# Kernel tuning notes

Measured on AMD Instinct MI355X. Metric: run time of the kernel, lower is better.

Reference implementation:

```python
import jax, jax.numpy as jnp
import numpy as np

B, S, D, H = 8, 1025, 768, 12
HD = D // H  # 64

def setup_inputs() -> dict:
    key = jax.random.key(0)
    ks = jax.random.split(key, 5)
    scale = 0.02
    return {
        "hidden_states": jax.random.normal(ks[0], (B, S, D), jnp.float32),
        "rel_bias": jax.random.normal(ks[1], (1, H, S, S), jnp.float32),
        "Wq": jax.random.normal(ks[2], (D, D), jnp.float32) * scale,
        "bq": jnp.zeros((D,), jnp.float32),
        "Wk": jax.random.normal(ks[3], (D, D), jnp.float32) * scale,
        "bk": jnp.zeros((D,), jnp.float32),
        "Wv": jax.random.normal(ks[4], (D, D), jnp.float32) * scale,
        "bv": jnp.zeros((D,), jnp.float32),
    }

def reference(hidden_states, rel_bias, Wq, bq, Wk, bk, Wv, bv):
    b, s, d = hidden_states.shape
    def split_heads(t):  # [B,S,D] -> [B,H,S,hd]
        return t.reshape(b, s, H, HD).transpose(0, 2, 1, 3)
    q = split_heads(hidden_states @ Wq + bq)
    k = split_heads(hidden_states @ Wk + bk)
    v = split_heads(hidden_states @ Wv + bv)
    inv_sqrt_hd = 1.0 / jnp.sqrt(jnp.asarray(HD, q.dtype))
    scores = jnp.einsum("bhqd,bhkd->bhqk", q, k) * inv_sqrt_hd
    scores = scores + rel_bias  # broadcast [1,H,S,S]
    probs = jax.nn.softmax(scores, axis=-1)
    ctx = jnp.einsum("bhqk,bhkd->bhqd", probs, v)
    out = ctx.transpose(0, 2, 1, 3).reshape(b, s, d)
    return out
```

## Files before the change

kernel.cpp:

```cpp
#include <hip/hip_runtime.h>

using f32x4  = __attribute__((ext_vector_type(4))) float;
using bf16x8 = __attribute__((ext_vector_type(8))) short;

#define SEQ 1025
#define NH  12

__device__ __forceinline__ unsigned short f2bf(float f) {
  unsigned u = __float_as_uint(f);
  u += 0x7FFFu + ((u >> 16) & 1u);
  return (unsigned short)(u >> 16);
}

__device__ __forceinline__ unsigned short f2bf_p(float f) {
  return (unsigned short)((__float_as_uint(f) + 0x8000u) >> 16);
}

__device__ __forceinline__ void async16(const void* g, void* s) {
  __builtin_amdgcn_global_load_lds(
      (const __attribute__((address_space(1))) void*)g,
      (__attribute__((address_space(3))) void*)s, 16, 0, 0);
}


__device__ __forceinline__ void conv_x_body(int bx, const float* __restrict__ X,
                                            ushort* __restrict__ Xb) {
  int t = bx * 256 + threadIdx.x;
  if (t >= 8320 * 96) return;
  int row = t / 96;
  size_t e = (size_t)t * 8;
  union { uint4 q; ushort us[8]; } o;
  if (row < 8200) {
    float4 f0 = *(const float4*)(X + e);
    float4 f1 = *(const float4*)(X + e + 4);
    o.us[0] = f2bf(f0.x); o.us[1] = f2bf(f0.y); o.us[2] = f2bf(f0.z); o.us[3] = f2bf(f0.w);
    o.us[4] = f2bf(f1.x); o.us[5] = f2bf(f1.y); o.us[6] = f2bf(f1.z); o.us[7] = f2bf(f1.w);
  } else {
    o.q = make_uint4(0, 0, 0, 0);
  }
  *(uint4*)(Xb + e) = o.q;
}

__device__ __forceinline__ void pack_w_body(int j, const float* __restrict__ Wq,
                                            const float* __restrict__ Wk,
                                            const float* __restrict__ Wv,
                                            ushort* __restrict__ Wt,
                                            const float* __restrict__ bq,
                                            const float* __restrict__ bk,
                                            const float* __restrict__ bv,
                                            float* __restrict__ bc,
                                            float (*tile)[33]) {
  const int nt = j % 72;
  const int kt = j / 72;
  if (kt == 0 && nt < 9) {
    int t2 = nt * 256 + threadIdx.x;
    if (t2 < 768) bc[t2] = bq[t2];
    else if (t2 < 1536) bc[t2] = bk[t2 - 768];
    else if (t2 < 2304) bc[t2] = bv[t2 - 1536];
  }
  const int sel = nt / 24;
  const int o0 = (nt - sel * 24) * 32;
  const int k0 = kt * 32;
  const float* W = sel == 0 ? Wq : sel == 1 ? Wk : Wv;
  const int t = threadIdx.x;
  const int x = t & 31, y = t >> 5;
  for (int p = 0; p < 4; ++p)
    tile[y + p * 8][x] = W[(size_t)(k0 + y + p * 8) * 768 + o0 + x];
  __syncthreads();
  for (int p = 0; p < 4; ++p) {
    const int nl = y + p * 8;
    Wt[(size_t)(nt * 32 + nl) * 768 + k0 + x] = f2bf(tile[x][nl]);
  }
}

__device__ __forceinline__ void repack_body(int id, const float* __restrict__ rel,
                                            float* __restrict__ bf,
                                            float (*lds)[580]) {
  const int half = id & 1;
  const int hw = id >> 1;
  const int h = hw / 72, w = hw - h * 72;
  const int t = threadIdx.x;
  const int W = half ? 512 : 576;
  const int cbase = half * 576;
  const float* src = rel + (size_t)h * SEQ * SEQ;
  for (int r = 0; r < 16; ++r) {
    int q = w * 16 + r; if (q > 1024) q = 1024;
    const float* row = src + (size_t)q * SEQ;
    for (int c = t; c < W; c += 256) {
      int col = cbase + c;
      lds[r][c] = (col <= 1024) ? row[col] * 1.44269504f : -3.0e30f;
    }
  }
  __syncthreads();
  const int lane = t >> 2, ct = t & 3;
  const int l16 = lane & 15, quad = lane >> 4;
  const int nkt = half ? 8 : 9;
  for (int ktl = 0; ktl < nkt; ++ktl) {
    const int kt = half * 9 + ktl;
    const int col = ktl * 64 + ct * 16 + l16;
    f32x4 v;
    v[0] = lds[quad * 4 + 0][col];
    v[1] = lds[quad * 4 + 1][col];
    v[2] = lds[quad * 4 + 2][col];
    v[3] = lds[quad * 4 + 3][col];
    *(f32x4*)(bf + (((size_t)h * 17 + kt) * 72 + w) * 1024 + lane * 16 + ct * 4) = v;
  }
}

__device__ __forceinline__ void gemm_body(int mb, int nb,
                                          const ushort* __restrict__ A,
                                          const ushort* __restrict__ Bt,
                                          const float* __restrict__ bias,
                                          ushort* __restrict__ Qo,
                                          ushort* __restrict__ Ko,
                                          ushort* __restrict__ Vo,
                                          char* smem) {
  ushort* a_sm = (ushort*)smem;
  ushort* b_sm = (ushort*)(smem + 8192);
  ushort* c_sm = (ushort*)(smem + 16384);
  const int t = threadIdx.x;
  const int lane = t & 63, wave = t >> 6;
  const int quad = lane >> 4, l16 = lane & 15;
  const int wrow = wave >> 1, wcol = wave & 1;
  const int m0 = mb * 128, n0 = nb * 128;

  f32x4 acc[4][4] = {};

  const ushort* a_g = A + (size_t)m0 * 768;
  const ushort* b_g = Bt + (size_t)n0 * 768;

  for (int k0 = 0; k0 < 768; k0 += 32) {
    __syncthreads();
    for (int r = 0; r < 2; ++r) {
      int c = r * 256 + t;
      int row = c >> 2;
      int colb = (c & 3) * 16;
      async16((const char*)(a_g + (size_t)row * 768 + k0) + colb, (char*)a_sm + c * 16);
      async16((const char*)(b_g + (size_t)row * 768 + k0) + colb, (char*)b_sm + c * 16);
    }
    __syncthreads();
    bf16x8 af[4], bfr[4];
    for (int i = 0; i < 4; ++i) {
      af[i]  = *(const bf16x8*)(a_sm + (wrow * 64 + i * 16 + l16) * 32 + quad * 8);
      bfr[i] = *(const bf16x8*)(b_sm + (wcol * 64 + i * 16 + l16) * 32 + quad * 8);
    }
    for (int i = 0; i < 4; ++i)
      for (int j = 0; j < 4; ++j)
        acc[i][j] = __builtin_amdgcn_mfma_f32_16x16x32_bf16(af[i], bfr[j], acc[i][j], 0, 0, 0);
  }

  const int sel = n0 / 768;
  const int o0 = n0 - sel * 768;
  const int hh0 = o0 >> 6;
  ushort* dst = sel == 0 ? Qo : sel == 1 ? Ko : Vo;
  float bvj[4];
  for (int j = 0; j < 4; ++j) bvj[j] = bias[n0 + wcol * 64 + j * 16 + l16];

  for (int p = 0; p < 2; ++p) {
    __syncthreads();
    if (wrow == p) {
      for (int i = 0; i < 4; ++i)
        for (int j = 0; j < 4; ++j)
          for (int r = 0; r < 4; ++r)
            c_sm[(i * 16 + quad * 4 + r) * 136 + wcol * 64 + j * 16 + l16] =
                f2bf(acc[i][j][r] + bvj[j]);
    }
    __syncthreads();
    const int head = t >> 7;
    const int ci = t & 127;
    for (int k = 0; k < 4; ++k) {
      int ch = ci + 128 * k;
      int row = ch >> 3, off = (ch & 7) * 8;
      int gm = m0 + p * 64 + row;
      if (gm < 8200) {
        int bb = gm / 1025, ss = gm - bb * 1025;
        uint4 v = *(const uint4*)(c_sm + row * 136 + head * 64 + off);
        *(uint4*)(dst + (((size_t)(bb * NH + hh0 + head) * SEQ + ss) << 6) + off) = v;
      }
    }
  }
}


__global__ __launch_bounds__(256) void prep(const float* __restrict__ X,
                                            ushort* __restrict__ Xb,
                                            const float* __restrict__ Wq,
                                            const float* __restrict__ Wk,
                                            const float* __restrict__ Wv,
                                            ushort* __restrict__ Wt,
                                            const float* __restrict__ bq,
                                            const float* __restrict__ bk,
                                            const float* __restrict__ bv,
                                            float* __restrict__ bc) {
  __shared__ __align__(16) float tile[32][33];
  const int bx = blockIdx.x;
  if (bx < 3120) conv_x_body(bx, X, Xb);
  else pack_w_body(bx - 3120, Wq, Wk, Wv, Wt, bq, bk, bv, bc, tile);
}

__global__ __launch_bounds__(256, 3) void gemm_repack(
    const ushort* __restrict__ A, const ushort* __restrict__ Bt,
    const float* __restrict__ biasc, ushort* __restrict__ Qo,
    ushort* __restrict__ Ko, ushort* __restrict__ Vo,
    const float* __restrict__ rel, float* __restrict__ bf) {
  __shared__ __align__(16) char smem[37120];
  const int bx = blockIdx.x;
  const int g = bx / 56, r = bx - g * 56;
  if (r < 24) {
    const int s = g * 24 + r;
    const int x = s & 7, k = s >> 3;
    const int ml = k / 18, n = k - ml * 18;
    int m;
    if (x == 0) m = ml;
    else { if (ml >= 8) return; m = 9 + (x - 1) * 8 + ml; }
    gemm_body(m, n, A, Bt, biasc, Qo, Ko, Vo, smem);
  } else {
    repack_body(g * 32 + (r - 24), rel, bf, (float(*)[580])smem);
  }
}

__global__ __launch_bounds__(256) void gemm_qkv_k(const ushort* __restrict__ A,
                                                  const ushort* __restrict__ Bt,
                                                  const float* __restrict__ biasc,
                                                  ushort* __restrict__ Qo,
                                                  ushort* __restrict__ Ko,
                                                  ushort* __restrict__ Vo) {
  __shared__ __align__(16) char smem[33792];
  gemm_body(blockIdx.x, blockIdx.y, A, Bt, biasc, Qo, Ko, Vo, smem);
}

__global__ __launch_bounds__(256, 4) void repack_k(const float* __restrict__ rel,
                                                   float* __restrict__ bf) {
  __shared__ __align__(16) float lds[16][580];
  repack_body(blockIdx.x, rel, bf, lds);
}

__global__ __launch_bounds__(256, 4) void attn(const ushort* __restrict__ Qb,
                                               const ushort* __restrict__ Kb,
                                               const ushort* __restrict__ Vb,
                                               const float* __restrict__ biasF,
                                               float* __restrict__ out) {
  __shared__ __align__(16) char smem[36864];
  ushort* p_sm = (ushort*)smem;
  ushort* k_sm = (ushort*)(smem + 18432);
  ushort* v_sm = (ushort*)(smem + 27648);

  const int t = threadIdx.x;
  const int lane = t & 63, wave = t >> 6;
  const int quad = lane >> 4, l16 = lane & 15;

  const int id = blockIdx.x;
  const int x = id & 7, s = id >> 3;
  const int Gg = s / 9, qt = s - Gg * 9;
  const int G = Gg * 8 + x;
  const int b = G / 12, h = G - b * 12;
  const int q0 = qt * 128;

  const size_t bh = (size_t)(b * NH + h) * SEQ * 64;
  const ushort* Qp = Qb + bh;
  const ushort* Kp = Kb + bh;
  const ushort* Vp = Vb + bh;

  uint4 kpre0, kpre1, vpre0, vpre1;
  const int vkp2 = t & 31, vhb = (t >> 5) * 8;

  auto issue_kv = [&](int kb) {
    {
      int c = t, row = c >> 3, cb = (c & 7) * 8;
      int rk = kb + row; if (rk > 1024) rk = 1024;
      kpre0 = *(const uint4*)(Kp + (size_t)rk * 64 + cb);
    }
    {
      int c = t + 256, row = c >> 3, cb = (c & 7) * 8;
      int rk = kb + row; if (rk > 1024) rk = 1024;
      kpre1 = *(const uint4*)(Kp + (size_t)rk * 64 + cb);
    }
    {
      int r0 = kb + vkp2 * 2;
      int r0c = r0 > 1024 ? 1024 : r0;
      int r1c = r0 + 1 > 1024 ? 1024 : r0 + 1;
      vpre0 = *(const uint4*)(Vp + (size_t)r0c * 64 + vhb);
      vpre1 = *(const uint4*)(Vp + (size_t)r1c * 64 + vhb);
    }
  };

  issue_kv(0);

  ushort* pw = p_sm + wave * (32 * 72);
  const int qbase = q0 + wave * 32;
  for (int i = 0; i < 4; ++i) {
    int c = lane + 64 * i;
    int row = c >> 3, cb = (c & 7) * 8;
    int rq = qbase + row; if (rq > 1024) rq = 1024;
    *(uint4*)(pw + row * 72 + cb) = *(const uint4*)(Qp + (size_t)rq * 64 + cb);
  }
  bf16x8 qf[2][2];
  for (int rt = 0; rt < 2; ++rt)
    for (int ks = 0; ks < 2; ++ks)
      qf[rt][ks] = *(const bf16x8*)(pw + (rt * 16 + l16) * 72 + ks * 32 + quad * 8);

  float lst[8] = {0, 0, 0, 0, 0, 0, 0, 0};
  f32x4 oacc[2][4] = {};
  const float c_scale = 0.18033688f;
  const float* bf_base = biasF +
      ((size_t)h * 17 * 72 + (qt * 8 + wave * 2)) * 1024 + (lane << 4);

  for (int kt = 0; kt < 17; ++kt) {
    __syncthreads();
    {
      int c = t;
      *(uint4*)(k_sm + (c >> 3) * 72 + (c & 7) * 8) = kpre0;
      c = t + 256;
      *(uint4*)(k_sm + (c >> 3) * 72 + (c & 7) * 8) = kpre1;
    }
    {
      union { uint4 q; ushort us[8]; } e0, e1;
      e0.q = vpre0; e1.q = vpre1;
      for (int e = 0; e < 8; ++e)
        *(unsigned*)(v_sm + (vhb + e) * 72 + vkp2 * 2) =
            (unsigned)e0.us[e] | ((unsigned)e1.us[e] << 16);
    }
    __syncthreads();

    const float* bfp = bf_base + (size_t)kt * (72 * 1024);
    f32x4 br[2][4];
    for (int rt = 0; rt < 2; ++rt)
      for (int ct = 0; ct < 4; ++ct)
        br[rt][ct] = *(const f32x4*)(bfp + rt * 1024 + ct * 4);

    if (kt < 16) issue_kv(kt * 64 + 64);

    f32x4 sc[2][4] = {};
    for (int ct = 0; ct < 4; ++ct)
      for (int ks = 0; ks < 2; ++ks) {
        bf16x8 kf = *(const bf16x8*)(k_sm + (ct * 16 + l16) * 72 + ks * 32 + quad * 8);
        sc[0][ct] = __builtin_amdgcn_mfma_f32_16x16x32_bf16(qf[0][ks], kf, sc[0][ct], 0, 0, 0);
        sc[1][ct] = __builtin_amdgcn_mfma_f32_16x16x32_bf16(qf[1][ks], kf, sc[1][ct], 0, 0, 0);
      }

    for (int rt = 0; rt < 2; ++rt)
      for (int ct = 0; ct < 4; ++ct)
        for (int r2 = 0; r2 < 4; ++r2) {
          float p = __builtin_amdgcn_exp2f(
              fmaf(sc[rt][ct][r2], c_scale, br[rt][ct][r2]));
          lst[rt * 4 + r2] += p;
          pw[(rt * 16 + quad * 4 + r2) * 72 + ct * 16 + l16] = f2bf_p(p);
        }

    for (int ks = 0; ks < 2; ++ks) {
      bf16x8 pf0 = *(const bf16x8*)(pw + l16 * 72 + ks * 32 + quad * 8);
      bf16x8 pf1 = *(const bf16x8*)(pw + (16 + l16) * 72 + ks * 32 + quad * 8);
      for (int c4 = 0; c4 < 4; ++c4) {
        bf16x8 vf = *(const bf16x8*)(v_sm + (c4 * 16 + l16) * 72 + ks * 32 + quad * 8);
        oacc[0][c4] = __builtin_amdgcn_mfma_f32_16x16x32_bf16(pf0, vf, oacc[0][c4], 0, 0, 0);
        oacc[1][c4] = __builtin_amdgcn_mfma_f32_16x16x32_bf16(pf1, vf, oacc[1][c4], 0, 0, 0);
      }
    }
  }

  for (int si = 0; si < 8; ++si) {
    float s2 = lst[si];
    s2 += __shfl_xor(s2, 1);
    s2 += __shfl_xor(s2, 2);
    s2 += __shfl_xor(s2, 4);
    s2 += __shfl_xor(s2, 8);
    lst[si] = s2;
  }
  for (int rt = 0; rt < 2; ++rt)
    for (int r2 = 0; r2 < 4; ++r2) {
      int sr = qbase + rt * 16 + quad * 4 + r2;
      if (sr < SEQ) {
        float inv = 1.0f / lst[rt * 4 + r2];
        float* op = out + ((size_t)b * SEQ + sr) * 768 + h * 64;
        for (int c4 = 0; c4 < 4; ++c4)
          op[c4 * 16 + l16] = oacc[rt][c4][r2] * inv;
      }
    }
}

extern "C" void kernel_launch(void* const* d_in, const int* in_sizes, int n_in,
                              void* d_out, int out_size, void* d_ws, size_t ws_size,
                              hipStream_t stream) {
  const float* X  = (const float*)d_in[0];
  const float* rb = (const float*)d_in[1];
  const float* Wq = (const float*)d_in[2];
  const float* bq = (const float*)d_in[3];
  const float* Wk = (const float*)d_in[4];
  const float* bk = (const float*)d_in[5];
  const float* Wv = (const float*)d_in[6];
  const float* bv = (const float*)d_in[7];
  float* out = (float*)d_out;
  char* ws = (char*)d_ws;

  ushort* Qb    = (ushort*)ws;
  ushort* Kb    = (ushort*)(ws + 12595200);
  ushort* Vb    = (ushort*)(ws + 25190400);
  ushort* Xb    = (ushort*)(ws + 37785600);
  ushort* Wt    = (ushort*)(ws + 50565120);
  float*  biasc = (float*)(ws + 54104064);

  const bool bigws = ws_size >= 114275328ULL;
  float* biasF = bigws ? (float*)(ws + 54113280) : (float*)(ws + 37785600);

  prep<<<3120 + 1728, 256, 0, stream>>>(X, Xb, Wq, Wk, Wv, Wt, bq, bk, bv, biasc);
  if (bigws) {
    gemm_repack<<<3024, 256, 0, stream>>>(Xb, Wt, biasc, Qb, Kb, Vb, rb, biasF);
  } else {
    gemm_qkv_k<<<dim3(65, 18), 256, 0, stream>>>(Xb, Wt, biasc, Qb, Kb, Vb);
    repack_k<<<NH * 72 * 2, 256, 0, stream>>>(rb, biasF);
  }
  attn<<<864, 256, 0, stream>>>(Qb, Kb, Vb, biasF, out);
}
```

Measured before the change: 308.9 us.

## Split fused prep/gemm-repack kernels and remap attention blocks for L2 locality

Undoes the fused prep and gemm+repack kernels and launches conv_x, pack_w, repack_k and a swizzled gemm_x as separate kernels. The attention block-to-(batch, head, q-tile) mapping is reordered so that consecutive blocks share a head's bias slice across batches, with a tail remap for the remaining tiles. The aim is better L2 reuse of the bias tensor in attention and simpler kernels, at the cost of extra launches and the lost overlap between the GEMM and the bias repack.

```diff
diff --git a/kernel.cpp b/kernel.cpp
--- a/kernel.cpp
+++ b/kernel.cpp
@@ -23,9 +23,9 @@
 }
 
 
-__device__ __forceinline__ void conv_x_body(int bx, const float* __restrict__ X,
-                                            ushort* __restrict__ Xb) {
-  int t = bx * 256 + threadIdx.x;
+__global__ __launch_bounds__(256) void conv_x(const float* __restrict__ X,
+                                              ushort* __restrict__ Xb) {
+  int t = blockIdx.x * 256 + threadIdx.x;
   if (t >= 8320 * 96) return;
   int row = t / 96;
   size_t e = (size_t)t * 8;
@@ -41,15 +41,16 @@
   *(uint4*)(Xb + e) = o.q;
 }
 
-__device__ __forceinline__ void pack_w_body(int j, const float* __restrict__ Wq,
-                                            const float* __restrict__ Wk,
-                                            const float* __restrict__ Wv,
-                                            ushort* __restrict__ Wt,
-                                            const float* __restrict__ bq,
-                                            const float* __restrict__ bk,
-                                            const float* __restrict__ bv,
-                                            float* __restrict__ bc,
-                                            float (*tile)[33]) {
+__global__ __launch_bounds__(256) void pack_w(const float* __restrict__ Wq,
+                                              const float* __restrict__ Wk,
+                                              const float* __restrict__ Wv,
+                                              ushort* __restrict__ Wt,
+                                              const float* __restrict__ bq,
+                                              const float* __restrict__ bk,
+                                              const float* __restrict__ bv,
+                                              float* __restrict__ bc) {
+  __shared__ __align__(16) float tile[32][33];
+  const int j = blockIdx.x;
   const int nt = j % 72;
   const int kt = j / 72;
   if (kt == 0 && nt < 9) {
@@ -73,9 +74,10 @@
   }
 }
 
-__device__ __forceinline__ void repack_body(int id, const float* __restrict__ rel,
-                                            float* __restrict__ bf,
-                                            float (*lds)[580]) {
+__global__ __launch_bounds__(256, 4) void repack_k(const float* __restrict__ rel,
+                                                   float* __restrict__ bf) {
+  __shared__ __align__(16) float lds[16][580];
+  const int id = blockIdx.x;
   const int half = id & 1;
   const int hw = id >> 1;
   const int h = hw / 72, w = hw - h * 72;
@@ -181,58 +183,20 @@
   }
 }
 
-
-__global__ __launch_bounds__(256) void prep(const float* __restrict__ X,
-                                            ushort* __restrict__ Xb,
-                                            const float* __restrict__ Wq,
-                                            const float* __restrict__ Wk,
-                                            const float* __restrict__ Wv,
-                                            ushort* __restrict__ Wt,
-                                            const float* __restrict__ bq,
-                                            const float* __restrict__ bk,
-                                            const float* __restrict__ bv,
-                                            float* __restrict__ bc) {
-  __shared__ __align__(16) float tile[32][33];
-  const int bx = blockIdx.x;
-  if (bx < 3120) conv_x_body(bx, X, Xb);
-  else pack_w_body(bx - 3120, Wq, Wk, Wv, Wt, bq, bk, bv, bc, tile);
-}
-
-__global__ __launch_bounds__(256, 3) void gemm_repack(
-    const ushort* __restrict__ A, const ushort* __restrict__ Bt,
-    const float* __restrict__ biasc, ushort* __restrict__ Qo,
-    ushort* __restrict__ Ko, ushort* __restrict__ Vo,
-    const float* __restrict__ rel, float* __restrict__ bf) {
-  __shared__ __align__(16) char smem[37120];
-  const int bx = blockIdx.x;
-  const int g = bx / 56, r = bx - g * 56;
-  if (r < 24) {
-    const int s = g * 24 + r;
-    const int x = s & 7, k = s >> 3;
-    const int ml = k / 18, n = k - ml * 18;
-    int m;
-    if (x == 0) m = ml;
-    else { if (ml >= 8) return; m = 9 + (x - 1) * 8 + ml; }
-    gemm_body(m, n, A, Bt, biasc, Qo, Ko, Vo, smem);
-  } else {
-    repack_body(g * 32 + (r - 24), rel, bf, (float(*)[580])smem);
-  }
-}
-
-__global__ __launch_bounds__(256) void gemm_qkv_k(const ushort* __restrict__ A,
-                                                  const ushort* __restrict__ Bt,
-                                                  const float* __restrict__ biasc,
-                                                  ushort* __restrict__ Qo,
-                                                  ushort* __restrict__ Ko,
-                                                  ushort* __restrict__ Vo) {
+__global__ __launch_bounds__(256) void gemm_x(const ushort* __restrict__ A,
+                                              const ushort* __restrict__ Bt,
+                                              const float* __restrict__ biasc,
+                                              ushort* __restrict__ Qo,
+                                              ushort* __restrict__ Ko,
+                                              ushort* __restrict__ Vo) {
   __shared__ __align__(16) char smem[33792];
-  gemm_body(blockIdx.x, blockIdx.y, A, Bt, biasc, Qo, Ko, Vo, smem);
-}
-
-__global__ __launch_bounds__(256, 4) void repack_k(const float* __restrict__ rel,
-                                                   float* __restrict__ bf) {
-  __shared__ __align__(16) float lds[16][580];
-  repack_body(blockIdx.x, rel, bf, lds);
+  const int s = blockIdx.x;
+  const int x = s & 7, k = s >> 3;
+  const int ml = k / 18, n = k - ml * 18;
+  int m;
+  if (x == 0) m = ml;
+  else { if (ml >= 8) return; m = 9 + (x - 1) * 8 + ml; }
+  gemm_body(m, n, A, Bt, biasc, Qo, Ko, Vo, smem);
 }
 
 __global__ __launch_bounds__(256, 4) void attn(const ushort* __restrict__ Qb,
@@ -250,10 +214,19 @@
   const int quad = lane >> 4, l16 = lane & 15;
 
   const int id = blockIdx.x;
-  const int x = id & 7, s = id >> 3;
-  const int Gg = s / 9, qt = s - Gg * 9;
-  const int G = Gg * 8 + x;
-  const int b = G / 12, h = G - b * 12;
+  int c, b;
+  if (id < 832) {
+    const int x = id & 7;
+    const int j = id >> 6;
+    b = (id >> 3) & 7;
+    c = j * 8 + x;
+  } else {
+    const int k = id - 832;
+    const int x = k & 7;
+    c = 104 + (x >> 1);
+    b = ((k >> 3) << 1) | (x & 1);
+  }
+  const int h = c / 9, qt = c - h * 9;
   const int q0 = qt * 128;
 
   const size_t bh = (size_t)(b * NH + h) * SEQ * 64;
@@ -266,12 +239,12 @@
 
   auto issue_kv = [&](int kb) {
     {
-      int c = t, row = c >> 3, cb = (c & 7) * 8;
+      int cc = t, row = cc >> 3, cb = (cc & 7) * 8;
       int rk = kb + row; if (rk > 1024) rk = 1024;
       kpre0 = *(const uint4*)(Kp + (size_t)rk * 64 + cb);
     }
     {
-      int c = t + 256, row = c >> 3, cb = (c & 7) * 8;
+      int cc = t + 256, row = cc >> 3, cb = (cc & 7) * 8;
       int rk = kb + row; if (rk > 1024) rk = 1024;
       kpre1 = *(const uint4*)(Kp + (size_t)rk * 64 + cb);
     }
@@ -289,8 +262,8 @@
   ushort* pw = p_sm + wave * (32 * 72);
   const int qbase = q0 + wave * 32;
   for (int i = 0; i < 4; ++i) {
-    int c = lane + 64 * i;
-    int row = c >> 3, cb = (c & 7) * 8;
+    int cc = lane + 64 * i;
+    int row = cc >> 3, cb = (cc & 7) * 8;
     int rq = qbase + row; if (rq > 1024) rq = 1024;
     *(uint4*)(pw + row * 72 + cb) = *(const uint4*)(Qp + (size_t)rq * 64 + cb);
   }
@@ -308,10 +281,10 @@
   for (int kt = 0; kt < 17; ++kt) {
     __syncthreads();
     {
-      int c = t;
-      *(uint4*)(k_sm + (c >> 3) * 72 + (c & 7) * 8) = kpre0;
-      c = t + 256;
-      *(uint4*)(k_sm + (c >> 3) * 72 + (c & 7) * 8) = kpre1;
+      int cc = t;
+      *(uint4*)(k_sm + (cc >> 3) * 72 + (cc & 7) * 8) = kpre0;
+      cc = t + 256;
+      *(uint4*)(k_sm + (cc >> 3) * 72 + (cc & 7) * 8) = kpre1;
     }
     {
       union { uint4 q; ushort us[8]; } e0, e1;
@@ -402,11 +375,13 @@
   const bool bigws = ws_size >= 114275328ULL;
   float* biasF = bigws ? (float*)(ws + 54113280) : (float*)(ws + 37785600);
 
-  prep<<<3120 + 1728, 256, 0, stream>>>(X, Xb, Wq, Wk, Wv, Wt, bq, bk, bv, biasc);
+  conv_x<<<3120, 256, 0, stream>>>(X, Xb);
+  pack_w<<<1728, 256, 0, stream>>>(Wq, Wk, Wv, Wt, bq, bk, bv, biasc);
   if (bigws) {
-    gemm_repack<<<3024, 256, 0, stream>>>(Xb, Wt, biasc, Qb, Kb, Vb, rb, biasF);
+    repack_k<<<NH * 72 * 2, 256, 0, stream>>>(rb, biasF);
+    gemm_x<<<1296, 256, 0, stream>>>(Xb, Wt, biasc, Qb, Kb, Vb);
   } else {
-    gemm_qkv_k<<<dim3(65, 18), 256, 0, stream>>>(Xb, Wt, biasc, Qb, Kb, Vb);
+    gemm_x<<<1296, 256, 0, stream>>>(Xb, Wt, biasc, Qb, Kb, Vb);
     repack_k<<<NH * 72 * 2, 256, 0, stream>>>(rb, biasF);
   }
   attn<<<864, 256, 0, stream>>>(Qb, Kb, Vb, biasF, out);
```

Result: slower. 322.9 us (+4.5%).
